# Kernel optimization log

Hardware: AMD Instinct MI355X
Metric: run time of the kernel (lower is better)

## Reference

```python
import jax, jax.numpy as jnp
import numpy as np

LAYERS, STACKS, K = 10, 3, 2
DILATIONS = [2 ** i for _ in range(STACKS) for i in range(LAYERS)]  # 30 layers


def conv1d(x, w, b=None, dilation=1):
    # x: [N, C_in, T], w: [C_out, C_in, K] (torch Conv1d layout), VALID padding
    out = jax.lax.conv_general_dilated(
        x, w, window_strides=(1,), padding='VALID',
        rhs_dilation=(dilation,), dimension_numbers=('NCH', 'OIH', 'NCH'))
    if b is not None:
        out = out + b[None, :, None]
    return out


def setup_inputs() -> dict:
    key = jax.random.key(0)
    ks = jax.random.split(key, 12)
    s = 0.1  # weight scale to avoid gate saturation
    return {
        'y': jax.random.normal(ks[0], (16, 1, 16384), dtype=jnp.float32),
        'causal_w': jax.random.normal(ks[1], (32, 1, 1), dtype=jnp.float32) * s,
        'causal_b': jax.random.normal(ks[2], (32,), dtype=jnp.float32) * s,
        'filt_w': jax.random.normal(ks[3], (30, 32, 32, K), dtype=jnp.float32) * s,
        'gate_w': jax.random.normal(ks[4], (30, 32, 32, K), dtype=jnp.float32) * s,
        'res_w': jax.random.normal(ks[5], (30, 32, 32, 1), dtype=jnp.float32) * s,
        'skip_w': jax.random.normal(ks[6], (30, 256, 32, 1), dtype=jnp.float32) * s,
        'end1_w': jax.random.normal(ks[7], (256, 256, 1), dtype=jnp.float32) * s,
        'end1_b': jax.random.normal(ks[8], (256,), dtype=jnp.float32) * s,
        'end2_w': jax.random.normal(ks[9], (256, 256, 1), dtype=jnp.float32) * s,
        'end2_b': jax.random.normal(ks[10], (256,), dtype=jnp.float32) * s,
    }


def reference(y, causal_w, causal_b, filt_w, gate_w, res_w, skip_w,
              end1_w, end1_b, end2_w, end2_b):
    x = conv1d(y, causal_w, causal_b)  # [B, 32, T]
    skip = None
    for i, d in enumerate(DILATIONS):
        r = x
        f = jnp.tanh(conv1d(x, filt_w[i], dilation=d))      # [B,32,T-d]
        g = jax.nn.sigmoid(conv1d(x, gate_w[i], dilation=d))
        x = f * g
        s = conv1d(x, skip_w[i])                             # [B,256,T-d]
        t = s.shape[-1]
        skip = s if skip is None else s + skip[:, :, -t:]
        x = conv1d(x, res_w[i])
        x = x + r[:, :, -x.shape[-1]:]
    x = jax.nn.relu(skip)
    x = jax.nn.relu(conv1d(x, end1_w, end1_b))
    x = conv1d(x, end2_w, end2_b)
    return x
```

## Files before the change

### kernel.cpp

```cpp
#include <hip/hip_runtime.h>
#include <hip/hip_bf16.h>
#include <cstdint>

#define NB 16
#define NC 32
#define T0 16384
#define NL 30
#define SKC 256
#define TF 13315
#define WGRP 192
#define XBC 320
#define XBS 20

typedef _Float16 f16;
typedef _Float16 f16x2 __attribute__((ext_vector_type(2)));
typedef _Float16 f16x8 __attribute__((ext_vector_type(8)));
typedef float f32x4 __attribute__((ext_vector_type(4)));
typedef uint32_t u32;

#define MFMA16(a,b,c) __builtin_amdgcn_mfma_f32_16x16x32_f16(a,b,c,0,0,0)

#define SCF (-2.88539008f)
#define SCG (-1.44269504f)
#define CLF 86.6f
#define CLG 43.3f

__device__ __forceinline__ float frcp(float x){
#if __has_builtin(__builtin_amdgcn_rcpf)
  return __builtin_amdgcn_rcpf(x);
#else
  return 1.f/x;
#endif
}
__device__ __forceinline__ float fexp2(float x){
#if __has_builtin(__builtin_amdgcn_exp2f)
  return __builtin_amdgcn_exp2f(x);
#else
  return exp2f(x);
#endif
}
__device__ __forceinline__ float clampf(float x, float c){
#if __has_builtin(__builtin_amdgcn_fmed3f)
  return __builtin_amdgcn_fmed3f(x, -c, c);
#else
  return fminf(fmaxf(x, -c), c);
#endif
}
__device__ __forceinline__ u32 pk2(float x, float y){
#if __has_builtin(__builtin_amdgcn_cvt_pkrtz)
  return __builtin_bit_cast(u32, __builtin_amdgcn_cvt_pkrtz(x, y));
#else
  f16x2 r; r.x = (f16)x; r.y = (f16)y;
  return __builtin_bit_cast(u32, r);
#endif
}
__device__ __forceinline__ u32 pkadd(u32 a, u32 b){
  f16x2 s = __builtin_bit_cast(f16x2, a) + __builtin_bit_cast(f16x2, b);
  return __builtin_bit_cast(u32, s);
}
#if __has_builtin(__builtin_amdgcn_global_load_lds)
#define HAVE_GLL 1
__device__ __forceinline__ void gll16(const void* g, void* l){
  __builtin_amdgcn_global_load_lds(
      (const __attribute__((address_space(1))) u32*)g,
      (__attribute__((address_space(3))) u32*)l, 16, 0, 0);
}
#else
#define HAVE_GLL 0
#endif
__device__ __forceinline__ size_t zfrag_off(int lz, int q){
  return (size_t)(lz & ~63)*NC + (size_t)(((lz>>4)&3)*512 + (q*16 + (lz&15))*8);
}
__device__ __forceinline__ int sigma_co(int q, int j){
  return (j < 4) ? (4*q + j) : (12 + 4*q + j);
}

__global__ __launch_bounds__(256) void prep3(
    const float* __restrict__ sw, const float* __restrict__ e1w,
    const float* __restrict__ e2w, const float* __restrict__ fw,
    const float* __restrict__ gw, const float* __restrict__ rw,
    f16* __restrict__ wsk, f16* __restrict__ e1f, f16* __restrict__ e2f,
    f16* __restrict__ fgpf, f16* __restrict__ ggpf, u32* __restrict__ rwp){
  int idx = blockIdx.x*256 + threadIdx.x;
  if (idx < 30720){
    int lane = idx & 63, mt = (idx>>6)&15, i = idx>>10;
    int m = mt*16 + (lane&15);
    int q = lane >> 4;
    const float* s = sw + ((size_t)i*SKC + m)*NC;
    f16* dp = wsk + (size_t)idx*8;
    #pragma unroll
    for (int j=0;j<8;j++) dp[j] = (f16)s[sigma_co(q, j)];
  } else if (idx < 38912){
    int j2 = idx - 30720;
    int lane = j2&63, mt = (j2>>6)&15, ks = j2>>10;
    int m = mt*16 + (lane&15);
    int k = ks*32 + (lane>>4)*8;
    const float* s = e1w + (size_t)m*SKC + k;
    f16* dp = e1f + (size_t)j2*8;
    #pragma unroll
    for (int j=0;j<8;j++) dp[j] = (f16)s[j];
  } else if (idx < 47104){
    int j2 = idx - 38912;
    int lane = j2&63, mt = (j2>>6)&15, ks = j2>>10;
    int m = mt*16 + (lane&15);
    int k = ks*32 + (lane>>4)*8;
    const float* s = e2w + (size_t)m*SKC + k;
    f16* dp = e2f + (size_t)j2*8;
    #pragma unroll
    for (int j=0;j<8;j++) dp[j] = (f16)s[j];
  } else if (idx < 77824){
    int j2 = idx - 47104;
    const float* s = fw + (size_t)j2*2;
    size_t base = (size_t)(j2 >> 5) * 64;
    int ci = j2 & 31;
    fgpf[base + ci]      = (f16)(s[0]*SCF);
    fgpf[base + 32 + ci] = (f16)(s[1]*SCF);
  } else if (idx < 108544){
    int j2 = idx - 77824;
    const float* s = gw + (size_t)j2*2;
    size_t base = (size_t)(j2 >> 5) * 64;
    int ci = j2 & 31;
    ggpf[base + ci]      = (f16)(s[0]*SCG);
    ggpf[base + 32 + ci] = (f16)(s[1]*SCG);
  } else if (idx < 123904){
    int j2 = idx - 108544;
    int i = j2 >> 9, c = (j2>>4)&31, pj = j2&15;
    const float* s = rw + ((size_t)i*NC + c)*NC;
    int q = pj >> 2, j0 = (2*pj) & 7;
    int c0 = sigma_co(q, j0);
    f16x2 p; p.x = (f16)s[c0]; p.y = (f16)s[c0+1];
    rwp[j2] = __builtin_bit_cast(u32, p);
  }
}

struct LW { f16x8 af[4]; f16x8 ag[4]; f16x8 ar[2]; };
__device__ __forceinline__ void lw_load(LW& w, const f16* __restrict__ fp,
    const f16* __restrict__ gp, const u32* __restrict__ rp, int lane){
  int m = lane & 15, q8 = (lane >> 4) * 8, q4 = (lane >> 4) * 4;
  #pragma unroll
  for (int mh = 0; mh < 2; mh++){
    #pragma unroll
    for (int tap = 0; tap < 2; tap++){
      w.af[mh*2+tap] = *(const f16x8*)&fp[((mh*16+m)*2+tap)*32 + q8];
      w.ag[mh*2+tap] = *(const f16x8*)&gp[((mh*16+m)*2+tap)*32 + q8];
    }
    w.ar[mh] = *(const f16x8*)&rp[(mh*16+m)*16 + q4];
  }
}

__device__ __forceinline__ void tile_core(const LW& w,
    uint4 a, uint4 b, uint2 rb0, uint2 rb1,
    uint4& zfrag, uint2& xo0, uint2& xo1){
  f16x8 A  = __builtin_bit_cast(f16x8, a);
  f16x8 Bt = __builtin_bit_cast(f16x8, b);
  f32x4 z4 = {0.f,0.f,0.f,0.f};
  f32x4 fa0 = MFMA16(w.af[0], A, z4); fa0 = MFMA16(w.af[1], Bt, fa0);
  f32x4 fa1 = MFMA16(w.af[2], A, z4); fa1 = MFMA16(w.af[3], Bt, fa1);
  f32x4 ga0 = MFMA16(w.ag[0], A, z4); ga0 = MFMA16(w.ag[1], Bt, ga0);
  f32x4 ga1 = MFMA16(w.ag[2], A, z4); ga1 = MFMA16(w.ag[3], Bt, ga1);
  u32 zq[4];
  #pragma unroll
  for (int mh = 0; mh < 2; mh++){
    f32x4 fv = mh ? fa1 : fa0;
    f32x4 gv = mh ? ga1 : ga0;
    float zz[4];
    #pragma unroll
    for (int r = 0; r < 4; r++){
      float t = fexp2(clampf(fv[r], CLF));
      float u = fexp2(clampf(gv[r], CLG));
      zz[r] = (1.f - t) * frcp((1.f + t) * (1.f + u));
    }
    zq[mh*2+0] = pk2(zz[0], zz[1]);
    zq[mh*2+1] = pk2(zz[2], zz[3]);
  }
  zfrag = make_uint4(zq[0], zq[1], zq[2], zq[3]);
  f16x8 zB = __builtin_bit_cast(f16x8, zfrag);
  f32x4 r0 = MFMA16(w.ar[0], zB, z4);
  f32x4 r1 = MFMA16(w.ar[1], zB, z4);
  xo0.x = pkadd(pk2(r0[0], r0[1]), rb0.x);
  xo0.y = pkadd(pk2(r0[2], r0[3]), rb0.y);
  xo1.x = pkadd(pk2(r1[0], r1[1]), rb1.x);
  xo1.y = pkadd(pk2(r1[2], r1[3]), rb1.y);
}

struct Trim7 { int t[7]; };

__global__ __launch_bounds__(256, 3) void group7m(
    const f16* __restrict__ xin, const float* __restrict__ y,
    const float* __restrict__ cw, const float* __restrict__ cb, int tc0,
    f16* __restrict__ xout, f16* __restrict__ zbase, int g0,
    int Lfinal, int TcAct, int zrows, int xpb,
    const f16* __restrict__ fgpf, const f16* __restrict__ ggpf,
    const u32* __restrict__ rwp, Trim7 trims){
  __shared__ u32 xb[2][XBC*XBS];
  int tid = threadIdx.x, b = blockIdx.y, o0 = blockIdx.x*WGRP;
  int lane = tid & 63, widx = tid >> 6;
  int Cf = Lfinal - o0; if (Cf > WGRP) Cf = WGRP;
  int Cin = Cf + 127;
  for (int p = tid; p < Cin; p += 256){
    u32* dst = &xb[0][p*XBS];
    if (y != nullptr){
      float yv = y[(size_t)b*T0 + tc0 + o0 + p];
      #pragma unroll
      for (int j = 0; j < 16; j++)
        dst[j] = pk2(fmaf(cw[2*j], yv, cb[2*j]), fmaf(cw[2*j+1], yv, cb[2*j+1]));
    } else {
      const uint4* src = (const uint4*)(xin + ((size_t)b*xpb + o0 + p)*NC);
      uint4* d4 = (uint4*)dst;
      d4[0]=src[0]; d4[1]=src[1]; d4[2]=src[2]; d4[3]=src[3];
    }
  }
  __syncthreads();
  int cur = 0;
  int tl = lane & 15, q = lane >> 4;
  size_t zlayer = (size_t)512*zrows;
  LW w;
  lw_load(w, fgpf + (size_t)g0*2048, ggpf + (size_t)g0*2048,
          rwp + (size_t)g0*512, lane);
  #pragma unroll 1
  for (int li = 0; li < 7; li++){
    int d = 1 << li;
    int count = Cf + 128 - (2 << li);
    LW wn;
    if (li < 6)
      lw_load(wn, fgpf + (size_t)(g0+li+1)*2048, ggpf + (size_t)(g0+li+1)*2048,
              rwp + (size_t)(g0+li+1)*512, lane);
    f16* zl = zbase + (size_t)(g0+li)*zlayer + (size_t)b*zrows*NC;
    int trim = trims.t[li];
    int ntiles = (count + 15) >> 4;
    for (int ti = widx; ti < ntiles; ti += 4){
      int c = ti*16 + tl;
      const u32* xc = &xb[cur][c*XBS];
      const u32* xd = &xb[cur][(c+d)*XBS];
      uint4 a  = *(const uint4*)&xc[q*4];
      uint4 b4 = *(const uint4*)&xd[q*4];
      uint2 rb0 = *(const uint2*)&xd[q*2];
      uint2 rb1 = *(const uint2*)&xd[8 + q*2];
      uint4 zf; uint2 xo0, xo1;
      tile_core(w, a, b4, rb0, rb1, zf, xo0, xo1);
      u32* xn = &xb[cur^1][c*XBS];
      *(uint2*)&xn[q*2] = xo0;
      *(uint2*)&xn[8 + q*2] = xo1;
      int lz = o0 + c - trim;
      if (c < count && lz >= 0 && lz < TcAct)
        *(uint4*)(zl + zfrag_off(lz, q)) = zf;
    }
    __syncthreads();
    if (li < 6) w = wn;
    cur ^= 1;
  }
  for (int p = tid; p < Cf; p += 256){
    const uint4* s4 = (const uint4*)&xb[cur][p*XBS];
    uint4* dd = (uint4*)(xout + ((size_t)b*xpb + o0 + p)*NC);
    dd[0]=s4[0]; dd[1]=s4[1]; dd[2]=s4[2]; dd[3]=s4[3];
  }
}

__global__ __launch_bounds__(256, 3) void singlem(
    const f16* __restrict__ xin, f16* __restrict__ xout, f16* __restrict__ zl,
    const f16* __restrict__ fp, const f16* __restrict__ gp,
    const u32* __restrict__ rp, int Tout, int d, int trim, int TcAct,
    int zrows, int xpb){
  int tid = threadIdx.x, b = blockIdx.y;
  int lane = tid & 63, widx = tid >> 6;
  int t0A = (blockIdx.x*8 + widx*2) * 16;
  if (t0A >= Tout) return;
  int haveB = (t0A + 16) < Tout;
  LW w;
  lw_load(w, fp, gp, rp, lane);
  int tl = lane & 15, q = lane >> 4;
  const f16* xbase = xin + (size_t)b*xpb*NC;
  int cA = t0A + tl;
  const f16* xcA = xbase + (size_t)cA*NC;
  const f16* xdA = xcA + (size_t)d*NC;
  uint4 aA  = *(const uint4*)(xcA + q*8);
  uint4 bA  = *(const uint4*)(xdA + q*8);
  uint2 r0A = *(const uint2*)(xdA + q*4);
  uint2 r1A = *(const uint2*)(xdA + 16 + q*4);
  int cB = cA + 16;
  const f16* xcB = xbase + (size_t)cB*NC;
  const f16* xdB = xcB + (size_t)d*NC;
  uint4 aB  = *(const uint4*)(xcB + q*8);
  uint4 bB  = *(const uint4*)(xdB + q*8);
  uint2 r0B = *(const uint2*)(xdB + q*4);
  uint2 r1B = *(const uint2*)(xdB + 16 + q*4);

  uint4 zfA, zfB; uint2 xo0A, xo1A, xo0B, xo1B;
  tile_core(w, aA, bA, r0A, r1A, zfA, xo0A, xo1A);
  tile_core(w, aB, bB, r0B, r1B, zfB, xo0B, xo1B);

  if (cA < Tout){
    f16* xoc = xout + ((size_t)b*xpb + cA)*NC;
    *(uint2*)(xoc + q*4) = xo0A;
    *(uint2*)(xoc + 16 + q*4) = xo1A;
  }
  if (haveB && cB < Tout){
    f16* xoc = xout + ((size_t)b*xpb + cB)*NC;
    *(uint2*)(xoc + q*4) = xo0B;
    *(uint2*)(xoc + 16 + q*4) = xo1B;
  }
  f16* zlb = zl + (size_t)b*zrows*NC;
  {
    int lz = cA - trim;
    if (cA < Tout && lz >= 0 && lz < TcAct)
      *(uint4*)(zlb + zfrag_off(lz, q)) = zfA;
  }
  if (haveB){
    int lz = cB - trim;
    if (cB < Tout && lz >= 0 && lz < TcAct)
      *(uint4*)(zlb + zfrag_off(lz, q)) = zfB;
  }
}

__global__ __launch_bounds__(512, 4) void skipend(
    const f16* __restrict__ zbase,
    const f16* __restrict__ wsk, const f16* __restrict__ e1f,
    const float* __restrict__ e1b, const f16* __restrict__ e2f,
    const float* __restrict__ e2b, float* __restrict__ out,
    int tc0, int TcAct, int zrows){
  __shared__ u32 smem[64*132];
  int tid = threadIdx.x, b = blockIdx.y, t0 = blockIdx.x*64;
  int w = tid>>6, lane = tid&63;
  int tl = lane & 15;
  int q  = lane >> 4;
  const uint4* wsk4 = (const uint4*)wsk;
  const uint4* e1f4 = (const uint4*)e1f;
  const uint4* e2f4 = (const uint4*)e2f;
  size_t zstepf = (size_t)512*zrows;
  const f16* zsrcb = zbase + ((size_t)b*zrows + t0)*NC;

  f32x4 acc[2][4];
  #pragma unroll
  for (int j=0;j<2;j++)
    #pragma unroll
    for (int tt=0;tt<4;tt++) acc[j][tt] = f32x4{0.f,0.f,0.f,0.f};

  auto stage = [&](int half, int lbase){
    #pragma unroll 1
    for (int s = w; s < 12; s += 8){
      int ks = s>>2, sq = s&3;
#if HAVE_GLL
      gll16(zsrcb + (size_t)(lbase+ks)*zstepf + (size_t)(sq*64+lane)*8,
            smem + (size_t)half*3072 + ks*1024 + sq*256);
#else
      uint4 v = *(const uint4*)(zsrcb + (size_t)(lbase+ks)*zstepf +
                                (size_t)(sq*64+lane)*8);
      *(uint4*)(smem + (size_t)half*3072 + ks*1024 + sq*256 + lane*4) = v;
#endif
    }
  };

  stage(0, 0);
  __syncthreads();
  #pragma unroll 1
  for (int g = 0; g < 10; g++){
    if (g < 9) stage((g+1)&1, 3*(g+1));
    const uint4* zr = (const uint4*)(smem + (size_t)(g&1)*3072);
    int lbase = g*3;
    #pragma unroll
    for (int k = 0; k < 3; k++){
      uint4 aw0 = wsk4[(size_t)(lbase+k)*1024 + (w*2+0)*64 + lane];
      uint4 aw1 = wsk4[(size_t)(lbase+k)*1024 + (w*2+1)*64 + lane];
      f16x8 zb0 = *(const f16x8*)&zr[k*256 + 0*64 + lane];
      f16x8 zb1 = *(const f16x8*)&zr[k*256 + 1*64 + lane];
      f16x8 zb2 = *(const f16x8*)&zr[k*256 + 2*64 + lane];
      f16x8 zb3 = *(const f16x8*)&zr[k*256 + 3*64 + lane];
      f16x8 a0 = __builtin_bit_cast(f16x8, aw0);
      f16x8 a1 = __builtin_bit_cast(f16x8, aw1);
      acc[0][0] = MFMA16(a0, zb0, acc[0][0]);
      acc[0][1] = MFMA16(a0, zb1, acc[0][1]);
      acc[0][2] = MFMA16(a0, zb2, acc[0][2]);
      acc[0][3] = MFMA16(a0, zb3, acc[0][3]);
      acc[1][0] = MFMA16(a1, zb0, acc[1][0]);
      acc[1][1] = MFMA16(a1, zb1, acc[1][1]);
      acc[1][2] = MFMA16(a1, zb2, acc[1][2]);
      acc[1][3] = MFMA16(a1, zb3, acc[1][3]);
    }
    __syncthreads();
  }
  int rq = q*4;
  #pragma unroll
  for (int j=0;j<2;j++){
    int c0 = (w*2+j)*16 + rq;
    #pragma unroll
    for (int tt=0;tt<4;tt++){
      int t = tt*16 + tl;
      u32 p0 = pk2(fmaxf(acc[j][tt][0],0.f), fmaxf(acc[j][tt][1],0.f));
      u32 p1 = pk2(fmaxf(acc[j][tt][2],0.f), fmaxf(acc[j][tt][3],0.f));
      *(uint2*)&smem[t*132 + (c0>>1)] = make_uint2(p0, p1);
    }
  }
  __syncthreads();
  #pragma unroll
  for (int j=0;j<2;j++)
    #pragma unroll
    for (int tt=0;tt<4;tt++) acc[j][tt] = f32x4{0.f,0.f,0.f,0.f};
  #pragma unroll
  for (int ks=0;ks<8;ks++){
    f16x8 zb[4];
    #pragma unroll
    for (int tt=0;tt<4;tt++)
      zb[tt] = *(const f16x8*)&smem[(tt*16+tl)*132 + ks*16 + q*4];
    #pragma unroll
    for (int j=0;j<2;j++){
      f16x8 a = __builtin_bit_cast(f16x8, e1f4[(size_t)(ks*16 + w*2+j)*64 + lane]);
      #pragma unroll
      for (int tt=0;tt<4;tt++)
        acc[j][tt] = MFMA16(a, zb[tt], acc[j][tt]);
    }
  }
  __syncthreads();
  #pragma unroll
  for (int j=0;j<2;j++){
    int c0 = (w*2+j)*16 + rq;
    float4 bv = *(const float4*)&e1b[c0];
    #pragma unroll
    for (int tt=0;tt<4;tt++){
      int t = tt*16 + tl;
      u32 p0 = pk2(fmaxf(acc[j][tt][0]+bv.x,0.f), fmaxf(acc[j][tt][1]+bv.y,0.f));
      u32 p1 = pk2(fmaxf(acc[j][tt][2]+bv.z,0.f), fmaxf(acc[j][tt][3]+bv.w,0.f));
      *(uint2*)&smem[t*132 + (c0>>1)] = make_uint2(p0, p1);
    }
  }
  __syncthreads();
  #pragma unroll
  for (int j=0;j<2;j++)
    #pragma unroll
    for (int tt=0;tt<4;tt++) acc[j][tt] = f32x4{0.f,0.f,0.f,0.f};
  #pragma unroll
  for (int ks=0;ks<8;ks++){
    f16x8 zb[4];
    #pragma unroll
    for (int tt=0;tt<4;tt++)
      zb[tt] = *(const f16x8*)&smem[(tt*16+tl)*132 + ks*16 + q*4];
    #pragma unroll
    for (int j=0;j<2;j++){
      f16x8 a = __builtin_bit_cast(f16x8, e2f4[(size_t)(ks*16 + w*2+j)*64 + lane]);
      #pragma unroll
      for (int tt=0;tt<4;tt++)
        acc[j][tt] = MFMA16(a, zb[tt], acc[j][tt]);
    }
  }
  __syncthreads();
  u32* slab = smem + (size_t)w*1024;
  int row = lane >> 2, cg = (lane & 3) * 16;
  #pragma unroll
  for (int j=0;j<2;j++){
    int c0 = (w*2+j)*16 + rq;
    float4 bv = *(const float4*)&e2b[c0];
    #pragma unroll
    for (int tt=0;tt<4;tt++){
      int t = tt*16 + tl;
      slab[(rq+0)*64 + t] = __builtin_bit_cast(u32, acc[j][tt][0] + bv.x);
      slab[(rq+1)*64 + t] = __builtin_bit_cast(u32, acc[j][tt][1] + bv.y);
      slab[(rq+2)*64 + t] = __builtin_bit_cast(u32, acc[j][tt][2] + bv.z);
      slab[(rq+3)*64 + t] = __builtin_bit_cast(u32, acc[j][tt][3] + bv.w);
    }
    int m0 = (w*2+j)*16;
    const uint4* sr = (const uint4*)(slab + row*64 + cg);
    uint4 v0 = sr[0], v1 = sr[1], v2 = sr[2], v3 = sr[3];
    float* op = out + ((size_t)b*SKC + m0 + row)*TF + tc0 + t0 + cg;
    if (t0 + 64 <= TcAct){
      *(uint4*)(op)    = v0;
      *(uint4*)(op+4)  = v1;
      *(uint4*)(op+8)  = v2;
      *(uint4*)(op+12) = v3;
    } else {
      u32 arr[16] = {v0.x,v0.y,v0.z,v0.w, v1.x,v1.y,v1.z,v1.w,
                     v2.x,v2.y,v2.z,v2.w, v3.x,v3.y,v3.z,v3.w};
      #pragma unroll
      for (int e = 0; e < 16; e++)
        if (t0 + cg + e < TcAct) op[e] = __builtin_bit_cast(float, arr[e]);
    }
  }
}

extern "C" void kernel_launch(void* const* d_in, const int* in_sizes, int n_in,
                              void* d_out, int out_size, void* d_ws, size_t ws_size,
                              hipStream_t stream) {
  (void)in_sizes; (void)n_in; (void)out_size;
  const float* y   = (const float*)d_in[0];
  const float* cw  = (const float*)d_in[1];
  const float* cb  = (const float*)d_in[2];
  const float* fw  = (const float*)d_in[3];
  const float* gw  = (const float*)d_in[4];
  const float* rw  = (const float*)d_in[5];
  const float* sw  = (const float*)d_in[6];
  const float* e1w = (const float*)d_in[7];
  const float* e1b = (const float*)d_in[8];
  const float* e2w = (const float*)d_in[9];
  const float* e2b = (const float*)d_in[10];
  float* out = (float*)d_out;
  char* ws = (char*)d_ws;

  const size_t fixedW = 1060864;
  int TCc = 0, xpb = 0;
  for (int c = 1; c <= 6; c++){
    int tcc = (((TF + c - 1)/c) + 63) & ~63;
    int xp  = tcc + 3264;
    size_t need = fixedW + 2*(size_t)xp*1024 + (size_t)NL*512*(size_t)tcc*2;
    if (need <= ws_size){ TCc = tcc; xpb = xp; break; }
  }
  if (!TCc){ TCc = 2240; xpb = 2240 + 3264; }

  f16* wsk   = (f16*)(ws);
  f16* e1f   = (f16*)(ws +   491520);
  f16* e2f   = (f16*)(ws +   622592);
  f16* fgpf  = (f16*)(ws +  753664);
  f16* ggpf  = (f16*)(ws +  876544);
  u32* rwp   = (u32*)(ws +  999424);
  f16* xpA   = (f16*)(ws + fixedW);
  f16* xpB   = (f16*)(ws + fixedW + (size_t)xpb*1024);
  f16* zstack = (f16*)(ws + fixedW + 2*(size_t)xpb*1024);

  int S[NL+1]; S[NL] = 0;
  for (int i = NL-1; i >= 0; i--) S[i] = S[i+1] + (1 << (i % 10));

  prep3<<<dim3(484), 256, 0, stream>>>(sw, e1w, e2w, fw, gw, rw,
                                       wsk, e1f, e2f, fgpf, ggpf, rwp);

  f16* bufs[2] = {xpA, xpB};
  for (int tc0 = 0; tc0 < TF; tc0 += TCc){
    int TcAct = TF - tc0; if (TcAct > TCc) TcAct = TCc;
    int cur = 0;
    for (int s = 0; s < 3; s++){
      int g0 = s*10;
      Trim7 tr;
      for (int li = 0; li < 7; li++) tr.t[li] = S[g0+li+1];
      int Lfinal = TcAct + S[g0+7];
      const f16* gin = (s == 0) ? (const f16*)nullptr : bufs[cur];
      const float* yArg = (s == 0) ? y : (const float*)nullptr;
      int nxt = (s == 0) ? 0 : (cur ^ 1);
      group7m<<<dim3((Lfinal + WGRP-1)/WGRP, NB), 256, 0, stream>>>(
          gin, yArg, cw, cb, tc0, bufs[nxt], zstack, g0, Lfinal, TcAct,
          TCc, xpb, fgpf, ggpf, rwp, tr);
      cur = nxt;
      for (int i = g0+7; i <= g0+9; i++){
        int d = 1 << (i % 10);
        int Tout = TcAct + S[i+1];
        singlem<<<dim3((Tout + 127)/128, NB), 256, 0, stream>>>(
            bufs[cur], bufs[cur^1], zstack + (size_t)i*512*TCc,
            fgpf + (size_t)i*2048, ggpf + (size_t)i*2048, rwp + (size_t)i*512,
            Tout, d, S[i+1], TcAct, TCc, xpb);
        cur ^= 1;
      }
    }
    skipend<<<dim3((TcAct + 63)/64, NB), 512, 0, stream>>>(
        zstack, wsk, e1f, e1b, e2f, e2b, out, tc0, TcAct, TCc);
  }
}
```

Baseline: 687.9 us.

## Reorder z stack so each 64-time block holds all layers contiguously

Changes the layout of the gated-activation stack from layer-major to batch/time-block-major with all 30 layers of a 64-step block stored contiguously. The skipend reduction over layers then streams one contiguous region per block instead of striding by a full layer plane, which should improve DRAM locality. It also pads the output transpose slab from a 64 to a 68-word stride to reduce LDS bank conflicts, which enlarges shared memory slightly. Writers in the layer kernels now scatter into more widely spaced addresses.

```diff
diff --git a/kernel.cpp b/kernel.cpp
--- a/kernel.cpp
+++ b/kernel.cpp
@@ -68,8 +68,9 @@
 #else
 #define HAVE_GLL 0
 #endif
-__device__ __forceinline__ size_t zfrag_off(int lz, int q){
-  return (size_t)(lz & ~63)*NC + (size_t)(((lz>>4)&3)*512 + (q*16 + (lz&15))*8);
+__device__ __forceinline__ size_t zfrag_off2(int b, int nblk, int l, int lz, int q){
+  return ((size_t)((b*nblk + (lz>>6))*NL + l))*2048
+       + (size_t)((((lz>>4)&3)*512) + (q*16 + (lz&15))*8);
 }
 __device__ __forceinline__ int sigma_co(int q, int j){
   return (j < 4) ? (4*q + j) : (12 + 4*q + j);
@@ -195,6 +196,7 @@
   __shared__ u32 xb[2][XBC*XBS];
   int tid = threadIdx.x, b = blockIdx.y, o0 = blockIdx.x*WGRP;
   int lane = tid & 63, widx = tid >> 6;
+  int nblk = zrows >> 6;
   int Cf = Lfinal - o0; if (Cf > WGRP) Cf = WGRP;
   int Cin = Cf + 127;
   for (int p = tid; p < Cin; p += 256){
@@ -213,7 +215,6 @@
   __syncthreads();
   int cur = 0;
   int tl = lane & 15, q = lane >> 4;
-  size_t zlayer = (size_t)512*zrows;
   LW w;
   lw_load(w, fgpf + (size_t)g0*2048, ggpf + (size_t)g0*2048,
           rwp + (size_t)g0*512, lane);
@@ -225,7 +226,6 @@
     if (li < 6)
       lw_load(wn, fgpf + (size_t)(g0+li+1)*2048, ggpf + (size_t)(g0+li+1)*2048,
               rwp + (size_t)(g0+li+1)*512, lane);
-    f16* zl = zbase + (size_t)(g0+li)*zlayer + (size_t)b*zrows*NC;
     int trim = trims.t[li];
     int ntiles = (count + 15) >> 4;
     for (int ti = widx; ti < ntiles; ti += 4){
@@ -243,7 +243,7 @@
       *(uint2*)&xn[8 + q*2] = xo1;
       int lz = o0 + c - trim;
       if (c < count && lz >= 0 && lz < TcAct)
-        *(uint4*)(zl + zfrag_off(lz, q)) = zf;
+        *(uint4*)(zbase + zfrag_off2(b, nblk, g0+li, lz, q)) = zf;
     }
     __syncthreads();
     if (li < 6) w = wn;
@@ -257,15 +257,16 @@
 }
 
 __global__ __launch_bounds__(256, 3) void singlem(
-    const f16* __restrict__ xin, f16* __restrict__ xout, f16* __restrict__ zl,
+    const f16* __restrict__ xin, f16* __restrict__ xout, f16* __restrict__ zbase,
     const f16* __restrict__ fp, const f16* __restrict__ gp,
     const u32* __restrict__ rp, int Tout, int d, int trim, int TcAct,
-    int zrows, int xpb){
+    int zrows, int xpb, int li){
   int tid = threadIdx.x, b = blockIdx.y;
   int lane = tid & 63, widx = tid >> 6;
   int t0A = (blockIdx.x*8 + widx*2) * 16;
   if (t0A >= Tout) return;
   int haveB = (t0A + 16) < Tout;
+  int nblk = zrows >> 6;
   LW w;
   lw_load(w, fp, gp, rp, lane);
   int tl = lane & 15, q = lane >> 4;
@@ -299,16 +300,15 @@
     *(uint2*)(xoc + q*4) = xo0B;
     *(uint2*)(xoc + 16 + q*4) = xo1B;
   }
-  f16* zlb = zl + (size_t)b*zrows*NC;
   {
     int lz = cA - trim;
     if (cA < Tout && lz >= 0 && lz < TcAct)
-      *(uint4*)(zlb + zfrag_off(lz, q)) = zfA;
+      *(uint4*)(zbase + zfrag_off2(b, nblk, li, lz, q)) = zfA;
   }
   if (haveB){
     int lz = cB - trim;
     if (cB < Tout && lz >= 0 && lz < TcAct)
-      *(uint4*)(zlb + zfrag_off(lz, q)) = zfB;
+      *(uint4*)(zbase + zfrag_off2(b, nblk, li, lz, q)) = zfB;
   }
 }
 
@@ -318,7 +318,7 @@
     const float* __restrict__ e1b, const f16* __restrict__ e2f,
     const float* __restrict__ e2b, float* __restrict__ out,
     int tc0, int TcAct, int zrows){
-  __shared__ u32 smem[64*132];
+  __shared__ u32 smem[8704];
   int tid = threadIdx.x, b = blockIdx.y, t0 = blockIdx.x*64;
   int w = tid>>6, lane = tid&63;
   int tl = lane & 15;
@@ -326,8 +326,8 @@
   const uint4* wsk4 = (const uint4*)wsk;
   const uint4* e1f4 = (const uint4*)e1f;
   const uint4* e2f4 = (const uint4*)e2f;
-  size_t zstepf = (size_t)512*zrows;
-  const f16* zsrcb = zbase + ((size_t)b*zrows + t0)*NC;
+  int nblk = zrows >> 6;
+  const f16* zb0 = zbase + ((size_t)((size_t)b*nblk + (t0>>6))*NL)*2048;
 
   f32x4 acc[2][4];
   #pragma unroll
@@ -340,11 +340,11 @@
     for (int s = w; s < 12; s += 8){
       int ks = s>>2, sq = s&3;
 #if HAVE_GLL
-      gll16(zsrcb + (size_t)(lbase+ks)*zstepf + (size_t)(sq*64+lane)*8,
+      gll16(zb0 + (size_t)(lbase+ks)*2048 + sq*512 + (size_t)lane*8,
             smem + (size_t)half*3072 + ks*1024 + sq*256);
 #else
-      uint4 v = *(const uint4*)(zsrcb + (size_t)(lbase+ks)*zstepf +
-                                (size_t)(sq*64+lane)*8);
+      uint4 v = *(const uint4*)(zb0 + (size_t)(lbase+ks)*2048 + sq*512 +
+                                (size_t)lane*8);
       *(uint4*)(smem + (size_t)half*3072 + ks*1024 + sq*256 + lane*4) = v;
 #endif
     }
@@ -361,20 +361,20 @@
     for (int k = 0; k < 3; k++){
       uint4 aw0 = wsk4[(size_t)(lbase+k)*1024 + (w*2+0)*64 + lane];
       uint4 aw1 = wsk4[(size_t)(lbase+k)*1024 + (w*2+1)*64 + lane];
-      f16x8 zb0 = *(const f16x8*)&zr[k*256 + 0*64 + lane];
-      f16x8 zb1 = *(const f16x8*)&zr[k*256 + 1*64 + lane];
-      f16x8 zb2 = *(const f16x8*)&zr[k*256 + 2*64 + lane];
-      f16x8 zb3 = *(const f16x8*)&zr[k*256 + 3*64 + lane];
+      f16x8 zb0f = *(const f16x8*)&zr[k*256 + 0*64 + lane];
+      f16x8 zb1f = *(const f16x8*)&zr[k*256 + 1*64 + lane];
+      f16x8 zb2f = *(const f16x8*)&zr[k*256 + 2*64 + lane];
+      f16x8 zb3f = *(const f16x8*)&zr[k*256 + 3*64 + lane];
       f16x8 a0 = __builtin_bit_cast(f16x8, aw0);
       f16x8 a1 = __builtin_bit_cast(f16x8, aw1);
-      acc[0][0] = MFMA16(a0, zb0, acc[0][0]);
-      acc[0][1] = MFMA16(a0, zb1, acc[0][1]);
-      acc[0][2] = MFMA16(a0, zb2, acc[0][2]);
-      acc[0][3] = MFMA16(a0, zb3, acc[0][3]);
-      acc[1][0] = MFMA16(a1, zb0, acc[1][0]);
-      acc[1][1] = MFMA16(a1, zb1, acc[1][1]);
-      acc[1][2] = MFMA16(a1, zb2, acc[1][2]);
-      acc[1][3] = MFMA16(a1, zb3, acc[1][3]);
+      acc[0][0] = MFMA16(a0, zb0f, acc[0][0]);
+      acc[0][1] = MFMA16(a0, zb1f, acc[0][1]);
+      acc[0][2] = MFMA16(a0, zb2f, acc[0][2]);
+      acc[0][3] = MFMA16(a0, zb3f, acc[0][3]);
+      acc[1][0] = MFMA16(a1, zb0f, acc[1][0]);
+      acc[1][1] = MFMA16(a1, zb1f, acc[1][1]);
+      acc[1][2] = MFMA16(a1, zb2f, acc[1][2]);
+      acc[1][3] = MFMA16(a1, zb3f, acc[1][3]);
     }
     __syncthreads();
   }
@@ -442,7 +442,7 @@
     }
   }
   __syncthreads();
-  u32* slab = smem + (size_t)w*1024;
+  u32* slab = smem + (size_t)w*1088;
   int row = lane >> 2, cg = (lane & 3) * 16;
   #pragma unroll
   for (int j=0;j<2;j++){
@@ -451,13 +451,13 @@
     #pragma unroll
     for (int tt=0;tt<4;tt++){
       int t = tt*16 + tl;
-      slab[(rq+0)*64 + t] = __builtin_bit_cast(u32, acc[j][tt][0] + bv.x);
-      slab[(rq+1)*64 + t] = __builtin_bit_cast(u32, acc[j][tt][1] + bv.y);
-      slab[(rq+2)*64 + t] = __builtin_bit_cast(u32, acc[j][tt][2] + bv.z);
-      slab[(rq+3)*64 + t] = __builtin_bit_cast(u32, acc[j][tt][3] + bv.w);
+      slab[(rq+0)*68 + t] = __builtin_bit_cast(u32, acc[j][tt][0] + bv.x);
+      slab[(rq+1)*68 + t] = __builtin_bit_cast(u32, acc[j][tt][1] + bv.y);
+      slab[(rq+2)*68 + t] = __builtin_bit_cast(u32, acc[j][tt][2] + bv.z);
+      slab[(rq+3)*68 + t] = __builtin_bit_cast(u32, acc[j][tt][3] + bv.w);
     }
     int m0 = (w*2+j)*16;
-    const uint4* sr = (const uint4*)(slab + row*64 + cg);
+    const uint4* sr = (const uint4*)(slab + row*68 + cg);
     uint4 v0 = sr[0], v1 = sr[1], v2 = sr[2], v3 = sr[3];
     float* op = out + ((size_t)b*SKC + m0 + row)*TF + tc0 + t0 + cg;
     if (t0 + 64 <= TcAct){
@@ -539,9 +539,9 @@
         int d = 1 << (i % 10);
         int Tout = TcAct + S[i+1];
         singlem<<<dim3((Tout + 127)/128, NB), 256, 0, stream>>>(
-            bufs[cur], bufs[cur^1], zstack + (size_t)i*512*TCc,
+            bufs[cur], bufs[cur^1], zstack,
             fgpf + (size_t)i*2048, ggpf + (size_t)i*2048, rwp + (size_t)i*512,
-            Tout, d, S[i+1], TcAct, TCc, xpb);
+            Tout, d, S[i+1], TcAct, TCc, xpb, i);
         cur ^= 1;
       }
     }
```

After: 688.5 us. About the same (+0.1%).
